# Performance work log

Hardware: AMD Instinct MI355X
Metric: run time of the kernel (lower is better)

Reference implementation:

```python
import jax, jax.numpy as jnp
import numpy as np

B, S, E, H = 2, 2048, 2048, 16
D = E // H

def setup_inputs() -> dict:
    key = jax.random.key(0)
    ks = jax.random.split(key, 9)
    sc = 1.0 / np.sqrt(E)
    return {
        "x":  jax.random.normal(ks[0], (B, S, E), jnp.float32),
        "Wq": jax.random.normal(ks[1], (E, E), jnp.float32) * sc,
        "bq": jax.random.normal(ks[2], (E,), jnp.float32) * 0.01,
        "Wk": jax.random.normal(ks[3], (E, E), jnp.float32) * sc,
        "bk": jax.random.normal(ks[4], (E,), jnp.float32) * 0.01,
        "Wv": jax.random.normal(ks[5], (E, E), jnp.float32) * sc,
        "bv": jax.random.normal(ks[6], (E,), jnp.float32) * 0.01,
        "Wo": jax.random.normal(ks[7], (E, E), jnp.float32) * sc,
        "bo": jax.random.normal(ks[8], (E,), jnp.float32) * 0.01,
    }

def _split_heads(t):
    # [B,S,E] -> [B,H,S,D]
    return t.reshape(B, S, H, D).transpose(0, 2, 1, 3)

def reference(x, Wq, bq, Wk, bk, Wv, bv, Wo, bo):
    # projections (nn.Linear: y = x @ W^T + b)
    q = _split_heads(x @ Wq.T + bq)
    k = _split_heads(x @ Wk.T + bk)
    v = _split_heads(x @ Wv.T + bv)

    # scaled causal attention; scale uses k.size(-1) == head_dim D
    scores = jnp.einsum("bhqd,bhkd->bhqk", q, k) / jnp.sqrt(jnp.asarray(D, q.dtype))
    causal = jnp.tril(jnp.ones((S, S), bool))  # [S,S]
    scores = jnp.where(causal[None, None, :, :], scores, -jnp.inf)
    # training path subtracts row max before softmax (no-op under stable softmax)
    scores = scores - jnp.max(scores, axis=-1, keepdims=True)
    attn = jax.nn.softmax(scores, axis=-1)
    # dropout_rate = 0.0 -> identity
    ctx = jnp.einsum("bhqk,bhkd->bhqd", attn, v)

    # merge heads [B,H,S,D] -> [B,S,E], final projection
    out = ctx.transpose(0, 2, 1, 3).reshape(B, S, E)
    return out @ Wo.T + bo
```

## Files before the change

kernel.cpp:

```cpp
#include <hip/hip_runtime.h>

typedef unsigned short u16;
typedef __attribute__((ext_vector_type(4))) float f32x4;
typedef __attribute__((ext_vector_type(8))) short s16x8;
typedef __attribute__((ext_vector_type(4))) unsigned short u16x4;

#define MFMA16(a, b, c) __builtin_amdgcn_mfma_f32_16x16x32_bf16((a), (b), (c), 0, 0, 0)

__device__ __forceinline__ u16 f2bf(float f) {
  union { float f; unsigned u; } v; v.f = f;
  unsigned u = v.u;
  u += 0x7fffu + ((u >> 16) & 1u);
  return (u16)(u >> 16);
}

__device__ __forceinline__ void gl_lds16(const void* g, void* l) {
  __builtin_amdgcn_global_load_lds(
      (const __attribute__((address_space(1))) void*)g,
      (__attribute__((address_space(3))) void*)l, 16, 0, 0);
}

__global__ void cast6(const float* __restrict__ x,
                      const float* __restrict__ w0, const float* __restrict__ w1,
                      const float* __restrict__ w2, const float* __restrict__ w3,
                      u16* __restrict__ ws) {
  const int y = blockIdx.y;
  const float* src;
  u16* dst;
  if (y < 2) { src = x + (size_t)y * 4194304; dst = ws + (size_t)y * 4194304; }
  else {
    src = (y == 2) ? w0 : (y == 3) ? w1 : (y == 4) ? w2 : w3;
    dst = ws + 8388608 + (size_t)(y - 2) * 4194304;
  }
  const int i = blockIdx.x * 256 + threadIdx.x;
  f32x4 v = ((const f32x4*)src)[i];
  u16x4 o;
#pragma unroll
  for (int e = 0; e < 4; ++e) o[e] = f2bf(v[e]);
  ((u16x4*)dst)[i] = o;
}

template <int SWAP>
__device__ __forceinline__ void gemm_core(const u16* __restrict__ A,
                                          const u16* __restrict__ Bw,
                                          u16* sA, u16* sB,
                                          f32x4 (&acc)[4][4],
                                          int m0, int n0, int tid) {
  const int lane = tid & 63, w = tid >> 6;
  const int ln = lane & 15, quad = lane >> 4, ln7 = ln & 7;
  const int wm = (w >> 1) * 64, wn = (w & 1) * 64;
  const int srow = lane >> 3;
  const int scol = (((lane & 7) ^ srow)) * 8;

  for (int k0 = 0; k0 < 2048; k0 += 64) {
#pragma unroll
    for (int c = 0; c < 4; ++c) {
      const int chunk = c * 4 + w;
      const int row = chunk * 8 + srow;
      gl_lds16(A + (size_t)(m0 + row) * 2048 + k0 + scol, (char*)sA + chunk * 1024);
      gl_lds16(Bw + (size_t)(n0 + row) * 2048 + k0 + scol, (char*)sB + chunk * 1024);
    }
    __syncthreads();
#pragma unroll
    for (int kk = 0; kk < 64; kk += 32) {
      s16x8 af[4], bf[4];
      const int g = (kk >> 3) + quad;
#pragma unroll
      for (int t = 0; t < 4; ++t) {
        af[t] = *(const s16x8*)&sA[(wm + t * 16 + ln) * 64 + ((g ^ ln7) << 3)];
        bf[t] = *(const s16x8*)&sB[(wn + t * 16 + ln) * 64 + ((g ^ ln7) << 3)];
      }
#pragma unroll
      for (int tm = 0; tm < 4; ++tm)
#pragma unroll
        for (int tn = 0; tn < 4; ++tn)
          acc[tm][tn] = SWAP ? MFMA16(bf[tn], af[tm], acc[tm][tn])
                             : MFMA16(af[tm], bf[tn], acc[tm][tn]);
    }
    __syncthreads();
  }
}

__global__ __launch_bounds__(512, 2) void gemm_qk256(
    const u16* __restrict__ A,
    const u16* __restrict__ W0, const u16* __restrict__ W1,
    const float* __restrict__ b0, const float* __restrict__ b1,
    u16* __restrict__ Qo, u16* __restrict__ Ko) {
  __shared__ __align__(16) u16 smem[65536];
  const int z = blockIdx.z;
  const u16* Bw = z ? W1 : W0;
  const float* bias = z ? b1 : b0;
  u16* out = z ? Ko : Qo;
  const float scale = z ? 1.0f : 0.08838834764831845f;

  const int tid = threadIdx.x;
  const int lane = tid & 63, w = tid >> 6;
  const int ln = lane & 15, quad = lane >> 4, ln7 = lane & 7;
  const int m0 = blockIdx.y * 256, n0 = blockIdx.x * 256;
  const int wm = (w >> 2) << 7, wn = (w & 3) << 6;

  const int ci0 = tid, ci1 = 512 + tid;
  const int r0 = ci0 >> 3, c0k = ((ci0 & 7) ^ (r0 & 7)) << 3;
  const int r1 = ci1 >> 3, c1k = ((ci1 & 7) ^ (r1 & 7)) << 3;
  const int abase = (w >> 2) << 13;
  const int bbase = 16384 + (((w >> 1) & 1) << 13) + ((w & 1) << 12);
  const int sw0 = (quad ^ ln7) << 3, sw1 = ((4 + quad) ^ ln7) << 3;

  f32x4 acc[8][4] = {};
  s16x8 af[8][2], bf[4][2];

  auto STGA = [&](int t) {
    u16* dst = smem + ((t & 1) << 15);
    const int kc = (t & 31) << 6;
    const u16* s0 = A + (size_t)(m0 + r0) * 2048 + kc + c0k;
    const u16* s1 = A + (size_t)(m0 + r1) * 2048 + kc + c1k;
    gl_lds16(s0, dst + ci0 * 8);
    gl_lds16(s1, dst + ci1 * 8);
    gl_lds16(s0 + (size_t)128 * 2048, dst + 8192 + ci0 * 8);
    gl_lds16(s1 + (size_t)128 * 2048, dst + 8192 + ci1 * 8);
  };
  auto STGB = [&](int t) {
    u16* dst = smem + ((t & 1) << 15) + 16384;
    const int kc = (t & 31) << 6;
    const u16* s0 = Bw + (size_t)(n0 + r0) * 2048 + kc + c0k;
    const u16* s1 = Bw + (size_t)(n0 + r1) * 2048 + kc + c1k;
    gl_lds16(s0, dst + ci0 * 8);
    gl_lds16(s1, dst + ci1 * 8);
    gl_lds16(s0 + (size_t)128 * 2048, dst + 8192 + ci0 * 8);
    gl_lds16(s1 + (size_t)128 * 2048, dst + 8192 + ci1 * 8);
  };
  auto RDA = [&](int buf, int tm0) {
    const u16* p = smem + (buf << 15) + abase;
#pragma unroll
    for (int u = 0; u < 4; ++u) {
      const int tt = tm0 + u;
      af[tt][0] = *(const s16x8*)&p[(tt * 16 + ln) * 64 + sw0];
      af[tt][1] = *(const s16x8*)&p[(tt * 16 + ln) * 64 + sw1];
    }
  };
  auto RDB = [&](int buf, int tn0) {
    const u16* p = smem + (buf << 15) + bbase;
#pragma unroll
    for (int u = 0; u < 2; ++u) {
      const int tt = tn0 + u;
      bf[tt][0] = *(const s16x8*)&p[(tt * 16 + ln) * 64 + sw0];
      bf[tt][1] = *(const s16x8*)&p[(tt * 16 + ln) * 64 + sw1];
    }
  };
  auto QM = [&](int tm0, int tn0) {
#pragma unroll
    for (int tm = tm0; tm < tm0 + 4; ++tm)
#pragma unroll
      for (int tn = tn0; tn < tn0 + 2; ++tn)
#pragma unroll
        for (int ks = 0; ks < 2; ++ks)
          acc[tm][tn] = MFMA16(bf[tn][ks], af[tm][ks], acc[tm][tn]);
  };

#define PH_MID()                                             \
  __builtin_amdgcn_s_barrier();                              \
  asm volatile("s_waitcnt lgkmcnt(0)" ::: "memory");         \
  __builtin_amdgcn_sched_barrier(0);                         \
  __builtin_amdgcn_s_setprio(1)
#define PH_END()                                             \
  __builtin_amdgcn_s_setprio(0);                             \
  __builtin_amdgcn_s_barrier()
#define PH_ENDV()                                            \
  __builtin_amdgcn_s_setprio(0);                             \
  asm volatile("s_waitcnt vmcnt(4)" ::: "memory");           \
  __builtin_amdgcn_s_barrier()

  STGA(0); STGB(0); STGA(1);
  asm volatile("s_waitcnt vmcnt(4)" ::: "memory");
  __builtin_amdgcn_s_barrier();

#pragma unroll 1
  for (int j = 0; j < 16; ++j) {
    const int t = 2 * j;
    RDA(0, 0); RDB(0, 0);
    STGB(t + 1);
    PH_MID(); QM(0, 0); PH_END();
    RDA(0, 4);
    PH_MID(); QM(4, 0); PH_END();
    RDB(0, 2);
    PH_MID(); QM(4, 2); PH_END();
    STGA(t + 2);
    PH_MID(); QM(0, 2); PH_ENDV();
    RDA(1, 0); RDB(1, 0);
    STGB(t + 2);
    PH_MID(); QM(0, 0); PH_END();
    RDA(1, 4);
    PH_MID(); QM(4, 0); PH_END();
    RDB(1, 2);
    PH_MID(); QM(4, 2); PH_END();
    STGA(t + 3);
    PH_MID(); QM(0, 2); PH_ENDV();
  }
  asm volatile("s_waitcnt vmcnt(0)" ::: "memory");
#undef PH_MID
#undef PH_END
#undef PH_ENDV

#pragma unroll
  for (int tn = 0; tn < 4; ++tn) {
    const int n_base = n0 + wn + tn * 16 + quad * 4;
    const f32x4 bv = *(const f32x4*)&bias[n_base];
    const int h = n_base >> 7, dl = n_base & 127;
#pragma unroll
    for (int tm = 0; tm < 8; ++tm) {
      const int m = m0 + wm + tm * 16 + ln;
      const int b = m >> 11, s = m & 2047;
      u16x4 ov;
#pragma unroll
      for (int r = 0; r < 4; ++r) ov[r] = f2bf((acc[tm][tn][r] + bv[r]) * scale);
      *(u16x4*)&out[(((size_t)(b * 16 + h)) << 18) + ((size_t)s << 7) + dl] = ov;
    }
  }
}

__global__ __launch_bounds__(256, 2) void gemm_v(const u16* __restrict__ A,
                                                 const u16* __restrict__ Bw,
                                                 const float* __restrict__ bias,
                                                 u16* __restrict__ Vo) {
  __shared__ __align__(16) u16 smem[16384];
  u16* sA = smem;
  u16* sB = smem + 8192;
  const int tid = threadIdx.x;
  const int lane = tid & 63, w = tid >> 6;
  const int ln = lane & 15, quad = lane >> 4;
  const int m0 = blockIdx.y * 128, n0 = blockIdx.x * 128;
  const int wm = (w >> 1) * 64, wn = (w & 1) * 64;

  f32x4 acc[4][4] = {};
  gemm_core<0>(A, Bw, sA, sB, acc, m0, n0, tid);
  const int b = m0 >> 11;
#pragma unroll
  for (int tn = 0; tn < 4; ++tn) {
    const int n = n0 + wn + tn * 16 + ln;
    const float bv = bias[n];
    const int h = n >> 7, dl = n & 127;
#pragma unroll
    for (int tm = 0; tm < 4; ++tm) {
      const int s_base = (m0 & 2047) + wm + tm * 16 + quad * 4;
      u16x4 ov;
#pragma unroll
      for (int r = 0; r < 4; ++r) ov[r] = f2bf(acc[tm][tn][r] + bv);
      *(u16x4*)&Vo[(((size_t)((b * 16 + h) * 128 + dl)) << 11) + s_base] = ov;
    }
  }
}

__global__ __launch_bounds__(256, 2) void gemm_out(const u16* __restrict__ A,
                                                   const u16* __restrict__ Bw,
                                                   const float* __restrict__ bias,
                                                   float* __restrict__ out) {
  __shared__ __align__(16) u16 smem[16384];
  u16* sA = smem;
  u16* sB = smem + 8192;
  const int tid = threadIdx.x;
  const int lane = tid & 63, w = tid >> 6;
  const int ln = lane & 15, quad = lane >> 4;
  const int m0 = blockIdx.y * 128, n0 = blockIdx.x * 128;
  const int wm = (w >> 1) * 64, wn = (w & 1) * 64;

  f32x4 acc[4][4] = {};
  gemm_core<1>(A, Bw, sA, sB, acc, m0, n0, tid);
#pragma unroll
  for (int tn = 0; tn < 4; ++tn) {
    const int n_base = n0 + wn + tn * 16 + quad * 4;
    const f32x4 bv = *(const f32x4*)&bias[n_base];
#pragma unroll
    for (int tm = 0; tm < 4; ++tm) {
      const int m = m0 + wm + tm * 16 + ln;
      f32x4 ov;
#pragma unroll
      for (int r = 0; r < 4; ++r) ov[r] = acc[tm][tn][r] + bv[r];
      *(f32x4*)&out[(size_t)m * 2048 + n_base] = ov;
    }
  }
}

__global__ __launch_bounds__(256, 2) void attn_kernel(const u16* __restrict__ Q,
                                                      const u16* __restrict__ Kp,
                                                      const u16* __restrict__ Vt,
                                                      u16* __restrict__ ctx) {
  __shared__ __align__(16) u16 smem[24576];
  u16* sP = smem;
  u16* sK = smem + 8192;
  u16* sV = smem + 16384;

  const int flat = blockIdx.x + (blockIdx.y << 4);
  const int bh = flat >> 4;
  const int i = (flat < 256) ? (15 - (flat & 15)) : (flat & 15);
  const size_t base = (size_t)bh << 18;

  const int tid = threadIdx.x, lane = tid & 63, w = tid >> 6;
  const int ln = lane & 15, quad = lane >> 4, ln7 = lane & 7;

#pragma unroll
  for (int c = 0; c < 8; ++c) {
    const int chunk0 = (c * 4 + w) * 64;
    const int chunk = chunk0 + lane;
    const int row = chunk >> 4, cc = chunk & 15;
    gl_lds16(Q + base + (size_t)((i * 128 + row) * 128 + ((cc ^ (row & 15)) << 3)),
             (char*)sK + chunk0 * 16);
  }
  __syncthreads();
  s16x8 qf[2][4];
#pragma unroll
  for (int qt = 0; qt < 2; ++qt)
#pragma unroll
    for (int kc = 0; kc < 4; ++kc)
      qf[qt][kc] =
          *(const s16x8*)&sK[(w * 32 + qt * 16 + ln) * 128 + (((kc * 4 + quad) ^ ln) << 3)];
  __syncthreads();

  auto stageK = [&](int j) {
#pragma unroll
    for (int c = 0; c < 4; ++c) {
      const int chunk0 = (c * 4 + w) * 64;
      const int chunk = chunk0 + lane;
      const int row = chunk >> 4, cc = chunk & 15;
      gl_lds16(Kp + base + (size_t)((j * 64 + row) * 128 + ((cc ^ (row & 15)) << 3)),
               (char*)sK + chunk0 * 16);
    }
  };
  auto stageV = [&](int j) {
#pragma unroll
    for (int c = 0; c < 4; ++c) {
      const int chunk0 = (c * 4 + w) * 64;
      const int chunk = chunk0 + lane;
      const int row = chunk >> 3, cc = chunk & 7;
      gl_lds16(Vt + base + (size_t)(row * 2048 + j * 64 + ((cc ^ (row & 7)) << 3)),
               (char*)sV + chunk0 * 16);
    }
  };

  stageK(0);
  stageV(0);
  __syncthreads();

  f32x4 o_acc[8][2] = {};
  float lsum[2] = {0.f, 0.f};
  const int jmax = 2 * i + 1;
  const int qg = i * 128 + w * 32 + ln;

  for (int j = 0; j <= jmax; ++j) {
    f32x4 sacc[4][2] = {};
#pragma unroll
    for (int kc = 0; kc < 4; ++kc) {
      s16x8 kf[4];
#pragma unroll
      for (int kt = 0; kt < 4; ++kt)
        kf[kt] = *(const s16x8*)&sK[(kt * 16 + ln) * 128 + (((kc * 4 + quad) ^ ln) << 3)];
#pragma unroll
      for (int kt = 0; kt < 4; ++kt)
#pragma unroll
        for (int qt = 0; qt < 2; ++qt)
          sacc[kt][qt] = MFMA16(kf[kt], qf[qt][kc], sacc[kt][qt]);
    }

    const bool diag = (j >= 2 * i);
#pragma unroll
    for (int kt = 0; kt < 4; ++kt)
#pragma unroll
      for (int qt = 0; qt < 2; ++qt) {
        u16x4 pk;
#pragma unroll
        for (int r = 0; r < 4; ++r) {
          const int kg = j * 64 + kt * 16 + quad * 4 + r;
          float pv = __expf(sacc[kt][qt][r]);
          if (diag && kg > qg + qt * 16) pv = 0.f;
          lsum[qt] += pv;
          pk[r] = f2bf(pv);
        }
        const int qrow = w * 32 + qt * 16 + ln;
        const int c = kt * 4 + quad;
        *(u16x4*)&sP[qrow * 64 + ((c ^ (qrow & 14)) << 2)] = pk;
      }
    __syncthreads();
    if (j < jmax) stageK(j + 1);

#pragma unroll
    for (int kc = 0; kc < 2; ++kc) {
      s16x8 vf[8], pf[2];
#pragma unroll
      for (int qt = 0; qt < 2; ++qt) {
        const int qrow = w * 32 + qt * 16 + ln;
        const int c0 = kc * 8 + quad * 2;
        pf[qt] = *(const s16x8*)&sP[qrow * 64 + ((c0 ^ (qrow & 14)) << 2)];
      }
#pragma unroll
      for (int dt = 0; dt < 8; ++dt)
        vf[dt] = *(const s16x8*)&sV[(dt * 16 + ln) * 64 + (((kc * 4 + quad) ^ ln7) << 3)];
#pragma unroll
      for (int dt = 0; dt < 8; ++dt)
#pragma unroll
        for (int qt = 0; qt < 2; ++qt)
          o_acc[dt][qt] = MFMA16(vf[dt], pf[qt], o_acc[dt][qt]);
    }
    __syncthreads();
    if (j < jmax) stageV(j + 1);
  }

  const int b = bh >> 4, h = bh & 15;
  float rinv[2];
#pragma unroll
  for (int qt = 0; qt < 2; ++qt) {
    float s = lsum[qt];
    s += __shfl_xor(s, 16);
    s += __shfl_xor(s, 32);
    rinv[qt] = __builtin_amdgcn_rcpf(s);
  }
#pragma unroll
  for (int dt = 0; dt < 8; ++dt)
#pragma unroll
    for (int qt = 0; qt < 2; ++qt) {
      const int sg = i * 128 + w * 32 + qt * 16 + ln;
      const int d0 = h * 128 + dt * 16 + quad * 4;
      u16x4 ov;
#pragma unroll
      for (int r = 0; r < 4; ++r) ov[r] = f2bf(o_acc[dt][qt][r] * rinv[qt]);
      *(u16x4*)&ctx[((size_t)b << 22) + (size_t)sg * 2048 + d0] = ov;
    }
}

extern "C" void kernel_launch(void* const* d_in, const int* in_sizes, int n_in,
                              void* d_out, int out_size, void* d_ws, size_t ws_size,
                              hipStream_t stream) {
  const float* x = (const float*)d_in[0];
  const float* Wq = (const float*)d_in[1];
  const float* bq = (const float*)d_in[2];
  const float* Wk = (const float*)d_in[3];
  const float* bk = (const float*)d_in[4];
  const float* Wv = (const float*)d_in[5];
  const float* bv = (const float*)d_in[6];
  const float* Wo = (const float*)d_in[7];
  const float* bo = (const float*)d_in[8];

  u16* ws = (u16*)d_ws;
  u16* xb = ws;
  u16* Wqb = xb + 8388608;
  u16* Wkb = Wqb + 4194304;
  u16* Wvb = Wkb + 4194304;
  u16* Wob = Wvb + 4194304;
  u16* Qb = Wob + 4194304;
  u16* Kb = Qb + 8388608;
  u16* Vtb = Kb + 8388608;
  u16* ctxb = Vtb + 8388608;

  cast6<<<dim3(4096, 6), 256, 0, stream>>>(x, Wq, Wk, Wv, Wo, ws);

  gemm_qk256<<<dim3(8, 16, 2), 512, 0, stream>>>(xb, Wqb, Wkb, bq, bk, Qb, Kb);
  gemm_v<<<dim3(16, 32), 256, 0, stream>>>(xb, Wvb, bv, Vtb);

  attn_kernel<<<dim3(16, 32), 256, 0, stream>>>(Qb, Kb, Vtb, ctxb);

  gemm_out<<<dim3(16, 32), 256, 0, stream>>>(ctxb, Wob, bo, (float*)d_out);
}
```

Before: 359.5 us.

## Software-pipeline LDS fragment reads one phase ahead of MFMA in GEMM loop

Restructures the GEMM main loop so LDS fragment reads and global-to-LDS stages for the next phase are issued right after the current phase's MFMAs, instead of waiting on lgkmcnt(0) behind a barrier before each MFMA block. Explicit lgkmcnt waits and sched_barriers are dropped so the compiler can interleave ds_reads with MFMA, and the partial vmcnt(4) waits become full vmcnt(0) seals. This aims to hide LDS latency, but the compiler now has to insert correct waits itself, and full vmcnt drains could stall on outstanding prefetches. Reads into the same fragment registers that are still being consumed could also create hazards or extra register pressure.

```diff
diff --git a/kernel.cpp b/kernel.cpp
--- a/kernel.cpp
+++ b/kernel.cpp
@@ -148,6 +148,7 @@
     }
   };
   auto QM = [&](int tm0, int tn0) {
+    __builtin_amdgcn_s_setprio(1);
 #pragma unroll
     for (int tm = tm0; tm < tm0 + 4; ++tm)
 #pragma unroll
@@ -155,51 +156,55 @@
 #pragma unroll
         for (int ks = 0; ks < 2; ++ks)
           acc[tm][tn] = MFMA16(bf[tn][ks], af[tm][ks], acc[tm][tn]);
-  };
-
-#define PH_MID()                                             \
-  __builtin_amdgcn_s_barrier();                              \
-  asm volatile("s_waitcnt lgkmcnt(0)" ::: "memory");         \
-  __builtin_amdgcn_sched_barrier(0);                         \
-  __builtin_amdgcn_s_setprio(1)
-#define PH_END()                                             \
-  __builtin_amdgcn_s_setprio(0);                             \
-  __builtin_amdgcn_s_barrier()
-#define PH_ENDV()                                            \
-  __builtin_amdgcn_s_setprio(0);                             \
-  asm volatile("s_waitcnt vmcnt(4)" ::: "memory");           \
-  __builtin_amdgcn_s_barrier()
+    __builtin_amdgcn_s_setprio(0);
+  };
+
+#define BAR()                                   \
+  asm volatile("" ::: "memory");                \
+  __builtin_amdgcn_s_barrier();                 \
+  asm volatile("" ::: "memory")
+#define SEAL() asm volatile("s_waitcnt vmcnt(0)" ::: "memory")
 
   STGA(0); STGB(0); STGA(1);
   asm volatile("s_waitcnt vmcnt(4)" ::: "memory");
-  __builtin_amdgcn_s_barrier();
+  BAR();
+  RDA(0, 0); RDB(0, 0);
 
 #pragma unroll 1
-  for (int j = 0; j < 16; ++j) {
-    const int t = 2 * j;
+  for (int u = 0; u < 16; ++u) {
+    const int t = 2 * u;
+    QM(0, 0);
+    RDA(0, 4);
+    STGB(t + 1);
+    BAR();
+    QM(4, 0);
+    RDB(0, 2);
+    BAR();
+    QM(4, 2);
+    SEAL();
+    BAR();
+    QM(0, 2);
+    RDA(1, 0); RDB(1, 0);
+    STGA(t + 2);
+    BAR();
+    QM(0, 0);
+    RDA(1, 4);
+    STGB(t + 2);
+    BAR();
+    QM(4, 0);
+    RDB(1, 2);
+    BAR();
+    QM(4, 2);
+    SEAL();
+    BAR();
+    QM(0, 2);
     RDA(0, 0); RDB(0, 0);
-    STGB(t + 1);
-    PH_MID(); QM(0, 0); PH_END();
-    RDA(0, 4);
-    PH_MID(); QM(4, 0); PH_END();
-    RDB(0, 2);
-    PH_MID(); QM(4, 2); PH_END();
-    STGA(t + 2);
-    PH_MID(); QM(0, 2); PH_ENDV();
-    RDA(1, 0); RDB(1, 0);
-    STGB(t + 2);
-    PH_MID(); QM(0, 0); PH_END();
-    RDA(1, 4);
-    PH_MID(); QM(4, 0); PH_END();
-    RDB(1, 2);
-    PH_MID(); QM(4, 2); PH_END();
     STGA(t + 3);
-    PH_MID(); QM(0, 2); PH_ENDV();
-  }
-  asm volatile("s_waitcnt vmcnt(0)" ::: "memory");
-#undef PH_MID
-#undef PH_END
-#undef PH_ENDV
+    BAR();
+  }
+  asm volatile("s_waitcnt vmcnt(0) lgkmcnt(0)" ::: "memory");
+#undef BAR
+#undef SEAL
 
 #pragma unroll
   for (int tn = 0; tn < 4; ++tn) {
```

After: 356.2 us. No clear change (-0.9%).
